# Performance work log

Hardware: AMD Instinct MI355X
Metric: run time of the kernel (lower is better)

Reference implementation:

```python
import jax, jax.numpy as jnp
import numpy as np

N_NODES = 15000
N_EDGES = 60000
NODE_VOCAB = 118 + 20000
EDGE_VOCAB = 4 + 50
NODE_INDIM = 64
EDGE_INDIM = 32
H = 32          # node_hidden_feats
EH = 64         # edge_hidden_feats
NUM_STEPS = 3   # num_step_message_passing
N_BOND_TYPES = 4  # edge ids < 4 are chemical bonds -> edge_func1, else knowledge relations -> edge_func2


def setup_inputs() -> dict:
    key = jax.random.key(0)
    ks = jax.random.split(key, 20)
    s = 0.05  # param scale for numerical stability
    return {
        "node_ids": jax.random.randint(ks[0], (N_NODES,), 0, NODE_VOCAB),
        "edge_ids": jax.random.randint(ks[1], (N_EDGES,), 0, EDGE_VOCAB),
        "src": jax.random.randint(ks[2], (N_EDGES,), 0, N_NODES),
        "dst": jax.random.randint(ks[3], (N_EDGES,), 0, N_NODES),
        "node_table": jax.random.normal(ks[4], (NODE_VOCAB, NODE_INDIM), jnp.float32),
        "edge_table": jax.random.normal(ks[5], (EDGE_VOCAB, EDGE_INDIM), jnp.float32),
        "proj_W": jax.random.normal(ks[6], (H, NODE_INDIM), jnp.float32) * s,
        "proj_b": jnp.zeros((H,), jnp.float32),
        "attn_w": jax.random.normal(ks[7], (2 * H,), jnp.float32) * s,
        "e1_W1": jax.random.normal(ks[8], (EH, EDGE_INDIM), jnp.float32) * s,
        "e1_b1": jnp.zeros((EH,), jnp.float32),
        "e1_W2": jax.random.normal(ks[9], (H * H, EH), jnp.float32) * s,
        "e1_b2": jnp.zeros((H * H,), jnp.float32),
        "e2_W1": jax.random.normal(ks[10], (EH, EDGE_INDIM), jnp.float32) * s,
        "e2_b1": jnp.zeros((EH,), jnp.float32),
        "e2_W2": jax.random.normal(ks[11], (H * H, EH), jnp.float32) * s,
        "e2_b2": jnp.zeros((H * H,), jnp.float32),
        "gru_Wih": jax.random.normal(ks[12], (3 * H, H), jnp.float32) * s,
        "gru_Whh": jax.random.normal(ks[13], (3 * H, H), jnp.float32) * s,
        "gru_bih": jnp.zeros((3 * H,), jnp.float32),
        "gru_bhh": jnp.zeros((3 * H,), jnp.float32),
    }


def _edge_softmax(logits, dst, num_nodes):
    # softmax over incoming edges of each destination node
    m = jax.ops.segment_max(logits, dst, num_segments=num_nodes)
    ex = jnp.exp(logits - m[dst])
    s = jax.ops.segment_sum(ex, dst, num_segments=num_nodes)
    return ex / s[dst]


def reference(node_ids, edge_ids, src, dst, node_table, edge_table, proj_W, proj_b,
              attn_w, e1_W1, e1_b1, e1_W2, e1_b2, e2_W1, e2_b1, e2_W2, e2_b2,
              gru_Wih, gru_Whh, gru_bih, gru_bhh):
    # --- embedding lookups ---
    nf = node_table[node_ids]                      # [N, node_indim]
    ef = edge_table[edge_ids]                      # [E, edge_indim]
    # --- project node feats: Linear + ReLU ---
    h = jax.nn.relu(nf @ proj_W.T + proj_b)        # [N, H]

    # --- per-edge weight matrices from the two edge MLPs (edge feats are
    # constant across message-passing steps, so compute once) ---
    def edge_mlp(W1, b1, W2, b2):
        z = jax.nn.relu(ef @ W1.T + b1)            # [E, EH]
        return (z @ W2.T + b2).reshape(-1, H, H)   # [E, H, H]

    W_e1 = edge_mlp(e1_W1, e1_b1, e1_W2, e1_b2)
    W_e2 = edge_mlp(e2_W1, e2_b1, e2_W2, e2_b2)
    is_bond = (edge_ids < N_BOND_TYPES)[:, None, None]
    W_edge = jnp.where(is_bond, W_e1, W_e2)        # [E, H, H]

    hidden = h                                     # GRU hidden state (seq of len 1 -> GRUCell)
    for _ in range(NUM_STEPS):
        # attention logits on edges: leaky_relu(attn_fc([h_src || h_dst]))
        a = jax.nn.leaky_relu(
            h[src] @ attn_w[:H] + h[dst] @ attn_w[H:])     # [E]
        alpha = _edge_softmax(a, dst, N_NODES)             # [E]
        # edge-conditioned message: (h_src @ W_e) weighted by attention
        msg = jnp.einsum('ei,eio->eo', h[src], W_edge) * alpha[:, None]  # [E, H]
        agg = jax.ops.segment_sum(msg, dst, num_segments=N_NODES)       # [N, H]
        m = jax.nn.relu(agg)
        # single GRU step (torch nn.GRU, 1 layer, seq_len 1)
        gi = m @ gru_Wih.T + gru_bih               # [N, 3H]
        gh = hidden @ gru_Whh.T + gru_bhh          # [N, 3H]
        ir, iz, inn = jnp.split(gi, 3, axis=1)
        hr, hz, hn = jnp.split(gh, 3, axis=1)
        r = jax.nn.sigmoid(ir + hr)
        z = jax.nn.sigmoid(iz + hz)
        n = jnp.tanh(inn + r * hn)
        hidden = (1.0 - z) * n + z * hidden
        h = hidden
    return h
```

## Files before the change

kernel.cpp:

```cpp
#include <hip/hip_runtime.h>
#include <hip/hip_bf16.h>
#include <math.h>

#define N_NODES   15000
#define N_EDGES   60000
#define EVOCAB    54
#define NODE_INDIM 64
#define EDGE_INDIM 32
#define H  32
#define EH 64
#define N_BOND 4

__global__ void edge_vocab_kernel(const float* __restrict__ edge_table,
                                  const float* __restrict__ e1_W1, const float* __restrict__ e1_b1,
                                  const float* __restrict__ e1_W2, const float* __restrict__ e1_b2,
                                  const float* __restrict__ e2_W1, const float* __restrict__ e2_b1,
                                  const float* __restrict__ e2_W2, const float* __restrict__ e2_b2,
                                  float* __restrict__ W_vocab) {
    int v = blockIdx.x;
    const float* W1 = (v < N_BOND) ? e1_W1 : e2_W1;
    const float* b1 = (v < N_BOND) ? e1_b1 : e2_b1;
    const float* W2 = (v < N_BOND) ? e1_W2 : e2_W2;
    const float* b2 = (v < N_BOND) ? e1_b2 : e2_b2;
    __shared__ float efs[EDGE_INDIM];
    __shared__ float zs[EH];
    int t = threadIdx.x;
    if (t < EDGE_INDIM) efs[t] = edge_table[v * EDGE_INDIM + t];
    __syncthreads();
    if (t < EH) {
        float acc = b1[t];
        #pragma unroll
        for (int j = 0; j < EDGE_INDIM; ++j) acc += efs[j] * W1[t * EDGE_INDIM + j];
        zs[t] = fmaxf(acc, 0.f);
    }
    __syncthreads();
    for (int o = t; o < H * H; o += blockDim.x) {
        float acc = b2[o];
        const float* w = W2 + o * EH;
        #pragma unroll
        for (int k = 0; k < EH; ++k) acc += zs[k] * w[k];
        W_vocab[v * H * H + o] = acc;
    }
}

__global__ void node_proj_kernel(const int* __restrict__ node_ids,
                                 const float* __restrict__ node_table,
                                 const float* __restrict__ proj_W,
                                 const float* __restrict__ proj_b,
                                 float* __restrict__ h) {
    __shared__ float Wl[H * (NODE_INDIM + 1)];
    __shared__ float nfl[8][NODE_INDIM];
    int t = threadIdx.x;
    for (int i = t; i < H * NODE_INDIM; i += 256)
        Wl[(i / NODE_INDIM) * (NODE_INDIM + 1) + (i % NODE_INDIM)] = proj_W[i];
    int ln = t >> 5, o = t & 31;
    int node = blockIdx.x * 8 + ln;
    int gid = node_ids[node];
    nfl[ln][o]      = node_table[gid * NODE_INDIM + o];
    nfl[ln][o + 32] = node_table[gid * NODE_INDIM + o + 32];
    __syncthreads();
    float acc = proj_b[o];
    #pragma unroll
    for (int j = 0; j < NODE_INDIM; ++j)
        acc += nfl[ln][j] * Wl[o * (NODE_INDIM + 1) + j];
    h[node * H + o] = fmaxf(acc, 0.f);
}

__global__ void attn_kernel(const int* __restrict__ src, const int* __restrict__ dst,
                            const float* __restrict__ h, const float* __restrict__ attn_w,
                            float* __restrict__ ex, float* __restrict__ sm) {
    int t = threadIdx.x;
    int sub = t >> 5, lane = t & 31;
    int e = blockIdx.x * 8 + sub;
    int s = src[e], d = dst[e];
    float val = h[s * H + lane] * attn_w[lane] + h[d * H + lane] * attn_w[H + lane];
    #pragma unroll
    for (int k = 16; k > 0; k >>= 1) val += __shfl_xor(val, k, 32);
    if (lane == 0) {
        float a = (val > 0.f) ? val : 0.01f * val;
        float ee = expf(a);
        ex[e] = ee;
        atomicAdd(&sm[d], ee);
    }
}

__global__ void msg_kernel(const int* __restrict__ src, const int* __restrict__ dst,
                           const int* __restrict__ edge_ids,
                           const float* __restrict__ h, const float* __restrict__ W_vocab,
                           const float* __restrict__ ex, const float* __restrict__ sm,
                           float* __restrict__ agg) {
    int t = threadIdx.x;
    int sub = t >> 5, o = t & 31;
    int e = blockIdx.x * 8 + sub;
    int s = src[e], d = dst[e], v = edge_ids[e];
    float hv = h[s * H + o];
    const float* W = W_vocab + v * H * H;
    float y = 0.f;
    #pragma unroll
    for (int i = 0; i < H; ++i)
        y += __shfl(hv, i, 32) * W[i * H + o];
    float alpha = ex[e] / sm[d];
    atomicAdd(&agg[d * H + o], alpha * y);
}

__global__ void gru_kernel(const float* __restrict__ agg,
                           const float* __restrict__ h_in,
                           const float* __restrict__ gWih, const float* __restrict__ gWhh,
                           const float* __restrict__ gbih, const float* __restrict__ gbhh,
                           float* __restrict__ h_out) {
    __shared__ float Wi[3 * H * (H + 1)];
    __shared__ float Wh[3 * H * (H + 1)];
    __shared__ float mt[8][H];
    __shared__ float ht[8][H];
    int t = threadIdx.x;
    for (int i = t; i < 3 * H * H; i += 256) {
        int r = i / H, c = i % H;
        Wi[r * (H + 1) + c] = gWih[i];
        Wh[r * (H + 1) + c] = gWhh[i];
    }
    int ln = t >> 5, o = t & 31;
    int node = blockIdx.x * 8 + ln;
    float m  = fmaxf(agg[node * H + o], 0.f);
    float hv = h_in[node * H + o];
    mt[ln][o] = m;
    ht[ln][o] = hv;
    __syncthreads();
    float gir = 0.f, giz = 0.f, gin = 0.f, ghr = 0.f, ghz = 0.f, ghn = 0.f;
    #pragma unroll
    for (int j = 0; j < H; ++j) {
        float mj = mt[ln][j], hj = ht[ln][j];
        gir += mj * Wi[(o)         * (H + 1) + j];
        giz += mj * Wi[(H + o)     * (H + 1) + j];
        gin += mj * Wi[(2 * H + o) * (H + 1) + j];
        ghr += hj * Wh[(o)         * (H + 1) + j];
        ghz += hj * Wh[(H + o)     * (H + 1) + j];
        ghn += hj * Wh[(2 * H + o) * (H + 1) + j];
    }
    float r = 1.f / (1.f + expf(-(gir + gbih[o]         + ghr + gbhh[o])));
    float z = 1.f / (1.f + expf(-(giz + gbih[H + o]     + ghz + gbhh[H + o])));
    float n = tanhf(gin + gbih[2 * H + o] + r * (ghn + gbhh[2 * H + o]));
    h_out[node * H + o] = (1.f - z) * n + z * hv;
}

extern "C" void kernel_launch(void* const* d_in, const int* in_sizes, int n_in,
                              void* d_out, int out_size, void* d_ws, size_t ws_size,
                              hipStream_t stream) {
    const int*   node_ids   = (const int*)d_in[0];
    const int*   edge_ids   = (const int*)d_in[1];
    const int*   src        = (const int*)d_in[2];
    const int*   dst        = (const int*)d_in[3];
    const float* node_table = (const float*)d_in[4];
    const float* edge_table = (const float*)d_in[5];
    const float* proj_W     = (const float*)d_in[6];
    const float* proj_b     = (const float*)d_in[7];
    const float* attn_w     = (const float*)d_in[8];
    const float* e1_W1      = (const float*)d_in[9];
    const float* e1_b1      = (const float*)d_in[10];
    const float* e1_W2      = (const float*)d_in[11];
    const float* e1_b2      = (const float*)d_in[12];
    const float* e2_W1      = (const float*)d_in[13];
    const float* e2_b1      = (const float*)d_in[14];
    const float* e2_W2      = (const float*)d_in[15];
    const float* e2_b2      = (const float*)d_in[16];
    const float* gWih       = (const float*)d_in[17];
    const float* gWhh       = (const float*)d_in[18];
    const float* gbih       = (const float*)d_in[19];
    const float* gbhh       = (const float*)d_in[20];

    char* ws = (char*)d_ws;
    float* W_vocab = (float*)(ws);
    float* h       = (float*)(ws + 221184);
    float* agg     = (float*)(ws + 221184 + 1920000);
    float* sm      = (float*)(ws + 221184 + 3840000);
    float* ex      = (float*)(ws + 221184 + 3900000);

    edge_vocab_kernel<<<EVOCAB, 256, 0, stream>>>(
        edge_table, e1_W1, e1_b1, e1_W2, e1_b2, e2_W1, e2_b1, e2_W2, e2_b2, W_vocab);
    node_proj_kernel<<<N_NODES / 8, 256, 0, stream>>>(
        node_ids, node_table, proj_W, proj_b, h);

    for (int step = 0; step < 3; ++step) {
        hipMemsetAsync(agg, 0, 1920000 + 60000, stream);
        attn_kernel<<<N_EDGES / 8, 256, 0, stream>>>(src, dst, h, attn_w, ex, sm);
        msg_kernel<<<N_EDGES / 8, 256, 0, stream>>>(src, dst, edge_ids, h, W_vocab, ex, sm, agg);
        float* hout = (step == 2) ? (float*)d_out : h;
        gru_kernel<<<N_NODES / 8, 256, 0, stream>>>(agg, h, gWih, gWhh, gbih, gbhh, hout);
    }
}
```

Baseline: 237.1 us.

## Fuse whole MPNN forward into one cooperative persistent kernel with deferred softmax normalization

Replaces the separate vocab, projection, attention, message, GRU and memset launches with a single cooperative kernel that uses grid-wide syncs between phases. Attention and message computation are merged into one edge pass: the unnormalized exp weight scales the message, and the softmax division by the per-node sum moves into the GRU phase. The edge weight tables are stored transposed so each lane reads float4 rows, and accumulators are cleared inside the GRU phase. This removes launch overhead, the ex buffer, and an extra gather pass over edges. In exchange it adds grid-sync costs and loses the shared-memory staging of GRU and projection weights.

```diff
diff --git a/kernel.cpp b/kernel.cpp
--- a/kernel.cpp
+++ b/kernel.cpp
@@ -1,6 +1,9 @@
 #include <hip/hip_runtime.h>
 #include <hip/hip_bf16.h>
+#include <hip/hip_cooperative_groups.h>
 #include <math.h>
+
+namespace cg = cooperative_groups;
 
 #define N_NODES   15000
 #define N_EDGES   60000
@@ -11,179 +14,156 @@
 #define EH 64
 #define N_BOND 4
 
-__global__ void edge_vocab_kernel(const float* __restrict__ edge_table,
-                                  const float* __restrict__ e1_W1, const float* __restrict__ e1_b1,
-                                  const float* __restrict__ e1_W2, const float* __restrict__ e1_b2,
-                                  const float* __restrict__ e2_W1, const float* __restrict__ e2_b1,
-                                  const float* __restrict__ e2_W2, const float* __restrict__ e2_b2,
-                                  float* __restrict__ W_vocab) {
-    int v = blockIdx.x;
-    const float* W1 = (v < N_BOND) ? e1_W1 : e2_W1;
-    const float* b1 = (v < N_BOND) ? e1_b1 : e2_b1;
-    const float* W2 = (v < N_BOND) ? e1_W2 : e2_W2;
-    const float* b2 = (v < N_BOND) ? e1_b2 : e2_b2;
-    __shared__ float efs[EDGE_INDIM];
-    __shared__ float zs[EH];
-    int t = threadIdx.x;
-    if (t < EDGE_INDIM) efs[t] = edge_table[v * EDGE_INDIM + t];
-    __syncthreads();
-    if (t < EH) {
-        float acc = b1[t];
-        #pragma unroll
-        for (int j = 0; j < EDGE_INDIM; ++j) acc += efs[j] * W1[t * EDGE_INDIM + j];
-        zs[t] = fmaxf(acc, 0.f);
+#define TASK_VOCAB  (EVOCAB * 1024)
+#define TASK_PROJ   (N_NODES * H)
+#define TASK_ZERO   ((N_NODES * H + N_NODES) / 4)
+#define TA (TASK_VOCAB + TASK_PROJ + TASK_ZERO)
+
+struct Params {
+    const int *node_ids, *edge_ids, *src, *dst;
+    const float *node_table, *edge_table, *proj_W, *proj_b, *attn_w;
+    const float *e1_W1, *e1_b1, *e1_W2, *e1_b2;
+    const float *e2_W1, *e2_b1, *e2_W2, *e2_b2;
+    const float *gWih, *gWhh, *gbih, *gbhh;
+    float *Wt;
+    float *h;
+    float *agg;
+    float *sm;
+    float *out;
+};
+
+__launch_bounds__(256, 2)
+__global__ void fused_mpnn(Params p) {
+    cg::grid_group grid = cg::this_grid();
+    const int tid = blockIdx.x * 256 + threadIdx.x;
+    const int NT  = gridDim.x * 256;
+
+    for (int t = tid; t < TA; t += NT) {
+        if (t < TASK_VOCAB) {
+            int v = t >> 10, f = t & 1023, l = t & 63;
+            const float* W1 = (v < N_BOND) ? p.e1_W1 : p.e2_W1;
+            const float* b1 = (v < N_BOND) ? p.e1_b1 : p.e2_b1;
+            const float* W2 = (v < N_BOND) ? p.e1_W2 : p.e2_W2;
+            const float* b2 = (v < N_BOND) ? p.e1_b2 : p.e2_b2;
+            const float* ef = p.edge_table + v * EDGE_INDIM;
+            float z = b1[l];
+            const float* w1r = W1 + l * EDGE_INDIM;
+            #pragma unroll
+            for (int j = 0; j < EDGE_INDIM; ++j) z += ef[j] * w1r[j];
+            z = fmaxf(z, 0.f);
+            float y = b2[f];
+            const float* w2r = W2 + f * EH;
+            #pragma unroll
+            for (int k = 0; k < EH; ++k) y += __shfl(z, k, 64) * w2r[k];
+            p.Wt[v * 1024 + (f & 31) * 32 + (f >> 5)] = y;
+        } else if (t < TASK_VOCAB + TASK_PROJ) {
+            int q = t - TASK_VOCAB;
+            int n = q >> 5, o = q & 31;
+            int gid = p.node_ids[n];
+            const float* nf = p.node_table + (size_t)gid * NODE_INDIM;
+            const float* wr = p.proj_W + o * NODE_INDIM;
+            float acc = p.proj_b[o];
+            #pragma unroll 8
+            for (int j = 0; j < NODE_INDIM; ++j) acc += nf[j] * wr[j];
+            p.h[q] = fmaxf(acc, 0.f);
+        } else {
+            int q = t - TASK_VOCAB - TASK_PROJ;
+            ((float4*)p.agg)[q] = make_float4(0.f, 0.f, 0.f, 0.f);
+        }
     }
-    __syncthreads();
-    for (int o = t; o < H * H; o += blockDim.x) {
-        float acc = b2[o];
-        const float* w = W2 + o * EH;
-        #pragma unroll
-        for (int k = 0; k < EH; ++k) acc += zs[k] * w[k];
-        W_vocab[v * H * H + o] = acc;
+    grid.sync();
+
+    for (int step = 0; step < 3; ++step) {
+        for (int t = tid; t < N_EDGES * 32; t += NT) {
+            int e = t >> 5, o = t & 31;
+            int s = p.src[e], d = p.dst[e], v = p.edge_ids[e];
+            float hs = p.h[s * 32 + o];
+            float hd = p.h[d * 32 + o];
+            float val = hs * p.attn_w[o] + hd * p.attn_w[32 + o];
+            #pragma unroll
+            for (int k = 16; k > 0; k >>= 1) val += __shfl_xor(val, k, 32);
+            float a  = (val > 0.f) ? val : 0.01f * val;
+            float ex = __expf(a);
+            const float4* W4 = (const float4*)(p.Wt + v * 1024 + o * 32);
+            float y = 0.f;
+            #pragma unroll
+            for (int ii = 0; ii < 8; ++ii) {
+                float4 w = W4[ii];
+                y += __shfl(hs, 4 * ii, 32)     * w.x;
+                y += __shfl(hs, 4 * ii + 1, 32) * w.y;
+                y += __shfl(hs, 4 * ii + 2, 32) * w.z;
+                y += __shfl(hs, 4 * ii + 3, 32) * w.w;
+            }
+            atomicAdd(&p.agg[d * 32 + o], ex * y);
+            if (o == 0) atomicAdd(&p.sm[d], ex);
+        }
+        grid.sync();
+
+        float* hout = (step == 2) ? p.out : p.h;
+        for (int t = tid; t < N_NODES * 32; t += NT) {
+            int n = t >> 5, o = t & 31;
+            float sinv = 1.f / p.sm[n];
+            float m  = fmaxf(p.agg[t] * sinv, 0.f);
+            float hv = p.h[t];
+            float gir = 0.f, giz = 0.f, gin = 0.f, ghr = 0.f, ghz = 0.f, ghn = 0.f;
+            const float* Wi0 = p.gWih + o * 32;
+            const float* Wi1 = p.gWih + (32 + o) * 32;
+            const float* Wi2 = p.gWih + (64 + o) * 32;
+            const float* Wh0 = p.gWhh + o * 32;
+            const float* Wh1 = p.gWhh + (32 + o) * 32;
+            const float* Wh2 = p.gWhh + (64 + o) * 32;
+            #pragma unroll 4
+            for (int j = 0; j < 32; ++j) {
+                float mj = __shfl(m, j, 32);
+                float hj = __shfl(hv, j, 32);
+                gir += mj * Wi0[j];  giz += mj * Wi1[j];  gin += mj * Wi2[j];
+                ghr += hj * Wh0[j];  ghz += hj * Wh1[j];  ghn += hj * Wh2[j];
+            }
+            float r = 1.f / (1.f + __expf(-(gir + p.gbih[o]      + ghr + p.gbhh[o])));
+            float z = 1.f / (1.f + __expf(-(giz + p.gbih[32 + o] + ghz + p.gbhh[32 + o])));
+            float nn = tanhf(gin + p.gbih[64 + o] + r * (ghn + p.gbhh[64 + o]));
+            hout[t] = (1.f - z) * nn + z * hv;
+            p.agg[t] = 0.f;
+            if (o == 0) p.sm[n] = 0.f;
+        }
+        grid.sync();
     }
-}
-
-__global__ void node_proj_kernel(const int* __restrict__ node_ids,
-                                 const float* __restrict__ node_table,
-                                 const float* __restrict__ proj_W,
-                                 const float* __restrict__ proj_b,
-                                 float* __restrict__ h) {
-    __shared__ float Wl[H * (NODE_INDIM + 1)];
-    __shared__ float nfl[8][NODE_INDIM];
-    int t = threadIdx.x;
-    for (int i = t; i < H * NODE_INDIM; i += 256)
-        Wl[(i / NODE_INDIM) * (NODE_INDIM + 1) + (i % NODE_INDIM)] = proj_W[i];
-    int ln = t >> 5, o = t & 31;
-    int node = blockIdx.x * 8 + ln;
-    int gid = node_ids[node];
-    nfl[ln][o]      = node_table[gid * NODE_INDIM + o];
-    nfl[ln][o + 32] = node_table[gid * NODE_INDIM + o + 32];
-    __syncthreads();
-    float acc = proj_b[o];
-    #pragma unroll
-    for (int j = 0; j < NODE_INDIM; ++j)
-        acc += nfl[ln][j] * Wl[o * (NODE_INDIM + 1) + j];
-    h[node * H + o] = fmaxf(acc, 0.f);
-}
-
-__global__ void attn_kernel(const int* __restrict__ src, const int* __restrict__ dst,
-                            const float* __restrict__ h, const float* __restrict__ attn_w,
-                            float* __restrict__ ex, float* __restrict__ sm) {
-    int t = threadIdx.x;
-    int sub = t >> 5, lane = t & 31;
-    int e = blockIdx.x * 8 + sub;
-    int s = src[e], d = dst[e];
-    float val = h[s * H + lane] * attn_w[lane] + h[d * H + lane] * attn_w[H + lane];
-    #pragma unroll
-    for (int k = 16; k > 0; k >>= 1) val += __shfl_xor(val, k, 32);
-    if (lane == 0) {
-        float a = (val > 0.f) ? val : 0.01f * val;
-        float ee = expf(a);
-        ex[e] = ee;
-        atomicAdd(&sm[d], ee);
-    }
-}
-
-__global__ void msg_kernel(const int* __restrict__ src, const int* __restrict__ dst,
-                           const int* __restrict__ edge_ids,
-                           const float* __restrict__ h, const float* __restrict__ W_vocab,
-                           const float* __restrict__ ex, const float* __restrict__ sm,
-                           float* __restrict__ agg) {
-    int t = threadIdx.x;
-    int sub = t >> 5, o = t & 31;
-    int e = blockIdx.x * 8 + sub;
-    int s = src[e], d = dst[e], v = edge_ids[e];
-    float hv = h[s * H + o];
-    const float* W = W_vocab + v * H * H;
-    float y = 0.f;
-    #pragma unroll
-    for (int i = 0; i < H; ++i)
-        y += __shfl(hv, i, 32) * W[i * H + o];
-    float alpha = ex[e] / sm[d];
-    atomicAdd(&agg[d * H + o], alpha * y);
-}
-
-__global__ void gru_kernel(const float* __restrict__ agg,
-                           const float* __restrict__ h_in,
-                           const float* __restrict__ gWih, const float* __restrict__ gWhh,
-                           const float* __restrict__ gbih, const float* __restrict__ gbhh,
-                           float* __restrict__ h_out) {
-    __shared__ float Wi[3 * H * (H + 1)];
-    __shared__ float Wh[3 * H * (H + 1)];
-    __shared__ float mt[8][H];
-    __shared__ float ht[8][H];
-    int t = threadIdx.x;
-    for (int i = t; i < 3 * H * H; i += 256) {
-        int r = i / H, c = i % H;
-        Wi[r * (H + 1) + c] = gWih[i];
-        Wh[r * (H + 1) + c] = gWhh[i];
-    }
-    int ln = t >> 5, o = t & 31;
-    int node = blockIdx.x * 8 + ln;
-    float m  = fmaxf(agg[node * H + o], 0.f);
-    float hv = h_in[node * H + o];
-    mt[ln][o] = m;
-    ht[ln][o] = hv;
-    __syncthreads();
-    float gir = 0.f, giz = 0.f, gin = 0.f, ghr = 0.f, ghz = 0.f, ghn = 0.f;
-    #pragma unroll
-    for (int j = 0; j < H; ++j) {
-        float mj = mt[ln][j], hj = ht[ln][j];
-        gir += mj * Wi[(o)         * (H + 1) + j];
-        giz += mj * Wi[(H + o)     * (H + 1) + j];
-        gin += mj * Wi[(2 * H + o) * (H + 1) + j];
-        ghr += hj * Wh[(o)         * (H + 1) + j];
-        ghz += hj * Wh[(H + o)     * (H + 1) + j];
-        ghn += hj * Wh[(2 * H + o) * (H + 1) + j];
-    }
-    float r = 1.f / (1.f + expf(-(gir + gbih[o]         + ghr + gbhh[o])));
-    float z = 1.f / (1.f + expf(-(giz + gbih[H + o]     + ghz + gbhh[H + o])));
-    float n = tanhf(gin + gbih[2 * H + o] + r * (ghn + gbhh[2 * H + o]));
-    h_out[node * H + o] = (1.f - z) * n + z * hv;
 }
 
 extern "C" void kernel_launch(void* const* d_in, const int* in_sizes, int n_in,
                               void* d_out, int out_size, void* d_ws, size_t ws_size,
                               hipStream_t stream) {
-    const int*   node_ids   = (const int*)d_in[0];
-    const int*   edge_ids   = (const int*)d_in[1];
-    const int*   src        = (const int*)d_in[2];
-    const int*   dst        = (const int*)d_in[3];
-    const float* node_table = (const float*)d_in[4];
-    const float* edge_table = (const float*)d_in[5];
-    const float* proj_W     = (const float*)d_in[6];
-    const float* proj_b     = (const float*)d_in[7];
-    const float* attn_w     = (const float*)d_in[8];
-    const float* e1_W1      = (const float*)d_in[9];
-    const float* e1_b1      = (const float*)d_in[10];
-    const float* e1_W2      = (const float*)d_in[11];
-    const float* e1_b2      = (const float*)d_in[12];
-    const float* e2_W1      = (const float*)d_in[13];
-    const float* e2_b1      = (const float*)d_in[14];
-    const float* e2_W2      = (const float*)d_in[15];
-    const float* e2_b2      = (const float*)d_in[16];
-    const float* gWih       = (const float*)d_in[17];
-    const float* gWhh       = (const float*)d_in[18];
-    const float* gbih       = (const float*)d_in[19];
-    const float* gbhh       = (const float*)d_in[20];
+    Params p;
+    p.node_ids   = (const int*)d_in[0];
+    p.edge_ids   = (const int*)d_in[1];
+    p.src        = (const int*)d_in[2];
+    p.dst        = (const int*)d_in[3];
+    p.node_table = (const float*)d_in[4];
+    p.edge_table = (const float*)d_in[5];
+    p.proj_W     = (const float*)d_in[6];
+    p.proj_b     = (const float*)d_in[7];
+    p.attn_w     = (const float*)d_in[8];
+    p.e1_W1 = (const float*)d_in[9];  p.e1_b1 = (const float*)d_in[10];
+    p.e1_W2 = (const float*)d_in[11]; p.e1_b2 = (const float*)d_in[12];
+    p.e2_W1 = (const float*)d_in[13]; p.e2_b1 = (const float*)d_in[14];
+    p.e2_W2 = (const float*)d_in[15]; p.e2_b2 = (const float*)d_in[16];
+    p.gWih  = (const float*)d_in[17]; p.gWhh  = (const float*)d_in[18];
+    p.gbih  = (const float*)d_in[19]; p.gbhh  = (const float*)d_in[20];
 
     char* ws = (char*)d_ws;
-    float* W_vocab = (float*)(ws);
-    float* h       = (float*)(ws + 221184);
-    float* agg     = (float*)(ws + 221184 + 1920000);
-    float* sm      = (float*)(ws + 221184 + 3840000);
-    float* ex      = (float*)(ws + 221184 + 3900000);
+    p.Wt  = (float*)(ws);
+    p.h   = (float*)(ws + 221184);
+    p.agg = (float*)(ws + 221184 + 1920000);
+    p.sm  = (float*)(ws + 221184 + 1920000 + 1920000);
+    p.out = (float*)d_out;
 
-    edge_vocab_kernel<<<EVOCAB, 256, 0, stream>>>(
-        edge_table, e1_W1, e1_b1, e1_W2, e1_b2, e2_W1, e2_b1, e2_W2, e2_b2, W_vocab);
-    node_proj_kernel<<<N_NODES / 8, 256, 0, stream>>>(
-        node_ids, node_table, proj_W, proj_b, h);
-
-    for (int step = 0; step < 3; ++step) {
-        hipMemsetAsync(agg, 0, 1920000 + 60000, stream);
-        attn_kernel<<<N_EDGES / 8, 256, 0, stream>>>(src, dst, h, attn_w, ex, sm);
-        msg_kernel<<<N_EDGES / 8, 256, 0, stream>>>(src, dst, edge_ids, h, W_vocab, ex, sm, agg);
-        float* hout = (step == 2) ? (float*)d_out : h;
-        gru_kernel<<<N_NODES / 8, 256, 0, stream>>>(agg, h, gWih, gWhh, gbih, gbhh, hout);
+    int maxb = 0;
+    int nblk = 512;
+    if (hipOccupancyMaxActiveBlocksPerMultiprocessor(&maxb, fused_mpnn, 256, 0) == hipSuccess
+        && maxb >= 1) {
+        int cap = maxb * 256;
+        if (nblk > cap) nblk = cap;
     }
+    void* kargs[] = { (void*)&p };
+    hipLaunchCooperativeKernel((void*)fused_mpnn, dim3(nblk), dim3(256), kargs, 0, stream);
 }
```

After: 776.3 us. +227.5%, slower.
